# Kernel optimization log

Measured on AMD Instinct MI355X. Metric: run time of the kernel, lower is better.

The kernel has to match this reference:

```python
import jax, jax.numpy as jnp
import numpy as np
import math

D_MODEL = 512
D_STATE = 16
D_CONV = 4
EXPAND = 2
D_INNER = EXPAND * D_MODEL          # 1024
D_HALF = D_INNER // 2               # 512, channels for x and z branches
DT_RANK = math.ceil(D_MODEL / 16)   # 32
B_SZ, L_SEQ = 8, 4096


def _dwconv_same(x, kern):
    """Depthwise 1D conv, TF 'same' padding, stride 1.
    x: (b, d, l); kern: (d, k). Returns (b, d, l)."""
    d = x.shape[1]
    w = kern[:, None, :]  # (O=d, I=1, K)
    return jax.lax.conv_general_dilated(
        x, w, window_strides=(1,), padding='SAME',
        dimension_numbers=('NCH', 'OIH', 'NCH'), feature_group_count=d)


def setup_inputs() -> dict:
    key = jax.random.key(0)
    ks = jax.random.split(key, 10)
    hidden_states = jax.random.normal(ks[0], (B_SZ, L_SEQ, D_MODEL), jnp.float32)
    W_in = jax.random.normal(ks[1], (D_MODEL, D_INNER), jnp.float32) * (D_MODEL ** -0.5)
    W_xproj = jax.random.normal(ks[2], (D_HALF, DT_RANK + 2 * D_STATE), jnp.float32) * (D_HALF ** -0.5)
    dt_init_std = DT_RANK ** -0.5
    W_dt = jax.random.uniform(ks[3], (DT_RANK, D_HALF), jnp.float32, -dt_init_std, dt_init_std)
    # bias init: inverse softplus of dt ~ LogUniform(1e-3, 0.1)
    dt = jnp.exp(jax.random.uniform(ks[4], (D_HALF,), jnp.float32,
                                    math.log(1e-3), math.log(0.1)))
    dt = jnp.clip(dt, 1e-4, 0.1)
    b_dt = dt + jnp.log(-jnp.expm1(-dt))
    A_log = jnp.log(jnp.broadcast_to(jnp.arange(1, D_STATE + 1, dtype=jnp.float32),
                                     (D_HALF, D_STATE)))
    D = jnp.ones((D_HALF,), jnp.float32)
    K_x = jax.random.normal(ks[5], (D_HALF, D_CONV), jnp.float32) * (D_CONV ** -0.5)
    K_z = jax.random.normal(ks[6], (D_HALF, D_CONV), jnp.float32) * (D_CONV ** -0.5)
    W_out = jax.random.normal(ks[7], (D_INNER, D_MODEL), jnp.float32) * (D_INNER ** -0.5)
    return {"hidden_states": hidden_states, "W_in": W_in, "W_xproj": W_xproj,
            "W_dt": W_dt, "b_dt": b_dt, "A_log": A_log, "D": D,
            "K_x": K_x, "K_z": K_z, "W_out": W_out}


def reference(hidden_states, W_in, W_xproj, W_dt, b_dt, A_log, D, K_x, K_z, W_out):
    r, n = W_dt.shape[0], A_log.shape[1]
    b, l, _ = hidden_states.shape
    xz = hidden_states @ W_in                         # (b,l,2d)
    x, z = jnp.split(xz, 2, axis=-1)                  # (b,l,d) each
    x = jax.nn.silu(_dwconv_same(x.transpose(0, 2, 1), K_x)).transpose(0, 2, 1)
    z = jax.nn.silu(_dwconv_same(z.transpose(0, 2, 1), K_z)).transpose(0, 2, 1)
    x_dbl = x @ W_xproj                               # (b,l,r+2n)
    delta = jax.nn.softplus(x_dbl[..., :r] @ W_dt + b_dt)   # (b,l,d)
    Bm = x_dbl[..., r:r + n]                          # (b,l,n)
    Cm = x_dbl[..., r + n:]                           # (b,l,n)
    A = -jnp.exp(A_log)                               # (d,n)

    def step(h, inp):
        x_t, d_t, B_t, C_t = inp                      # (b,d),(b,d),(b,n),(b,n)
        dA = jnp.exp(d_t[:, :, None] * A)             # (b,d,n)
        h = h * dA + (d_t * x_t)[:, :, None] * B_t[:, None, :]
        y_t = jnp.einsum('bdn,bn->bd', h, C_t)
        return h, y_t

    xs = (x.transpose(1, 0, 2), delta.transpose(1, 0, 2),
          Bm.transpose(1, 0, 2), Cm.transpose(1, 0, 2))
    h0 = jnp.zeros((b, x.shape[-1], n), x.dtype)
    _, ys = jax.lax.scan(step, h0, xs)                # (l,b,d)
    y = ys.transpose(1, 0, 2) + x * D                 # skip term D*x
    out = jnp.concatenate([y, z], axis=-1) @ W_out    # (b,l,d_model)
    return out
```

## Files before the change

### kernel.cpp

```cpp
#include <hip/hip_runtime.h>
#include <hip/hip_bf16.h>
#include <cstdint>
#include <cstddef>

#define B_SZ    8
#define L_SEQ   4096
#define D_MODEL 512
#define D_INNER 1024
#define D_HALF  512
#define DT_RANK 32
#define N_STATE 16
#define M_ROWS  (B_SZ * L_SEQ)
#define N_CHUNK 64
#define L_CHK   64

typedef __hip_bfloat16 bf16;
typedef __attribute__((ext_vector_type(8))) short bf16x8;
typedef __attribute__((ext_vector_type(4))) float f32x4;

__device__ __forceinline__ void unpack8(uint4 v, float* f) {
  f[0] = __uint_as_float(v.x << 16); f[1] = __uint_as_float(v.x & 0xffff0000u);
  f[2] = __uint_as_float(v.y << 16); f[3] = __uint_as_float(v.y & 0xffff0000u);
  f[4] = __uint_as_float(v.z << 16); f[5] = __uint_as_float(v.z & 0xffff0000u);
  f[6] = __uint_as_float(v.w << 16); f[7] = __uint_as_float(v.w & 0xffff0000u);
}
__device__ __forceinline__ unsigned pack2(float a, float b) {
  bf16 ha = __float2bfloat16(a), hb = __float2bfloat16(b);
  return (unsigned)*(const unsigned short*)&ha |
         ((unsigned)*(const unsigned short*)&hb << 16);
}

typedef __attribute__((address_space(1))) const void gas_void;
typedef __attribute__((address_space(3))) void las_void;
__device__ __forceinline__ void gload_lds16(const void* g, void* l) {
  __builtin_amdgcn_global_load_lds((gas_void*)g, (las_void*)l, 16, 0, 0);
}

template <bool AF32>
__global__ __launch_bounds__(256)
void gemm_mfma(const void* __restrict__ A1v, const bf16* __restrict__ A2,
               const bf16* __restrict__ BT, bf16* __restrict__ C,
               float* __restrict__ Cf, int N, int K) {
  __shared__ bf16 As[2][128 * 32];
  __shared__ bf16 Bs[2][128 * 32];
  const int tid  = threadIdx.x;
  const int bm   = blockIdx.x * 128;
  const int bn   = blockIdx.y * 128;
  const int wave = tid >> 6;
  const int lane = tid & 63;
  const int wm   = (wave & 1) * 64;
  const int wn   = (wave >> 1) * 64;
  const int l15  = lane & 15;
  const int quad = lane >> 4;
  const int lr   = lane >> 2;
  const int lc   = (lane & 3) * 8;

  f32x4 acc[4][4] = {};
  const int NT = K >> 5;

  auto stage = [&](int buf, int t) {
    const int k0 = t * 32;
#pragma unroll
    for (int p = 0; p < 2; ++p) {
      const int c = wave + p * 4;
      gload_lds16(&BT[(size_t)(bn + c * 16 + lr) * K + k0 + lc],
                  &Bs[buf][c * 16 * 32]);
    }
    if constexpr (AF32) {
      const float* Ap = (const float*)A1v;
      const int sr0 = tid >> 2;
      const int sc  = (tid & 3) * 8;
#pragma unroll
      for (int p = 0; p < 2; ++p) {
        const int r = sr0 + p * 64;
        const float* s = &Ap[(size_t)(bm + r) * 512 + k0 + sc];
        const float4 v0 = *(const float4*)s;
        const float4 v1 = *(const float4*)(s + 4);
        uint4 o;
        o.x = pack2(v0.x, v0.y); o.y = pack2(v0.z, v0.w);
        o.z = pack2(v1.x, v1.y); o.w = pack2(v1.z, v1.w);
        *(uint4*)&As[buf][r * 32 + sc] = o;
      }
    } else {
      const bf16* Ap = (k0 < 512) ? (const bf16*)A1v : A2;
      const int ka = k0 & 511;
#pragma unroll
      for (int p = 0; p < 2; ++p) {
        const int c = wave + p * 4;
        gload_lds16(&Ap[(size_t)(bm + c * 16 + lr) * 512 + ka + lc],
                    &As[buf][c * 16 * 32]);
      }
    }
  };

  stage(0, 0);
  __syncthreads();
  int cur = 0;
  for (int t = 0; t < NT; ++t) {
    if (t + 1 < NT) stage(cur ^ 1, t + 1);
    bf16x8 af[4], bfr[4];
#pragma unroll
    for (int i = 0; i < 4; ++i)
      af[i] = *(const bf16x8*)&As[cur][(wm + i * 16 + l15) * 32 + quad * 8];
#pragma unroll
    for (int j = 0; j < 4; ++j)
      bfr[j] = *(const bf16x8*)&Bs[cur][(wn + j * 16 + l15) * 32 + quad * 8];
#pragma unroll
    for (int i = 0; i < 4; ++i)
#pragma unroll
      for (int j = 0; j < 4; ++j)
        acc[i][j] = __builtin_amdgcn_mfma_f32_16x16x32_bf16(
            af[i], bfr[j], acc[i][j], 0, 0, 0);
    __syncthreads();
    cur ^= 1;
  }

  if (Cf) {
#pragma unroll
    for (int i = 0; i < 4; ++i)
#pragma unroll
      for (int j = 0; j < 4; ++j)
#pragma unroll
        for (int r = 0; r < 4; ++r) {
          const int row = bm + wm + i * 16 + quad * 4 + r;
          const int col = bn + wn + j * 16 + l15;
          Cf[(size_t)row * N + col] = acc[i][j][r];
        }
  } else {
#pragma unroll
    for (int i = 0; i < 4; ++i)
#pragma unroll
      for (int j = 0; j < 4; ++j)
#pragma unroll
        for (int r = 0; r < 4; ++r) {
          const int row = bm + wm + i * 16 + quad * 4 + r;
          const int col = bn + wn + j * 16 + l15;
          C[(size_t)row * N + col] = __float2bfloat16(acc[i][j][r]);
        }
  }
}

__global__ __launch_bounds__(256)
void gemm_xproj(const bf16* __restrict__ A, const bf16* __restrict__ BT,
                float* __restrict__ C, bf16* __restrict__ dtA) {
  __shared__ bf16 As[2][128 * 32];
  __shared__ bf16 Bs[2][64 * 32];
  const int tid  = threadIdx.x;
  const int bm   = blockIdx.x * 128;
  const int wave = tid >> 6;
  const int lane = tid & 63;
  const int wm   = (wave & 1) * 64;
  const int wn   = (wave >> 1) * 32;
  const int l15  = lane & 15;
  const int quad = lane >> 4;
  const int lr   = lane >> 2;
  const int lc   = (lane & 3) * 8;

  f32x4 acc[4][2] = {};

  auto stage = [&](int buf, int t) {
    const int k0 = t * 32;
#pragma unroll
    for (int p = 0; p < 2; ++p) {
      const int c = wave + p * 4;
      gload_lds16(&A[(size_t)(bm + c * 16 + lr) * 512 + k0 + lc],
                  &As[buf][c * 16 * 32]);
    }
    gload_lds16(&BT[(size_t)(wave * 16 + lr) * 512 + k0 + lc],
                &Bs[buf][wave * 16 * 32]);
  };

  stage(0, 0);
  __syncthreads();
  int cur = 0;
  for (int t = 0; t < 16; ++t) {
    if (t + 1 < 16) stage(cur ^ 1, t + 1);
    bf16x8 af[4], bfr[2];
#pragma unroll
    for (int i = 0; i < 4; ++i)
      af[i] = *(const bf16x8*)&As[cur][(wm + i * 16 + l15) * 32 + quad * 8];
#pragma unroll
    for (int j = 0; j < 2; ++j)
      bfr[j] = *(const bf16x8*)&Bs[cur][(wn + j * 16 + l15) * 32 + quad * 8];
#pragma unroll
    for (int i = 0; i < 4; ++i)
#pragma unroll
      for (int j = 0; j < 2; ++j)
        acc[i][j] = __builtin_amdgcn_mfma_f32_16x16x32_bf16(
            af[i], bfr[j], acc[i][j], 0, 0, 0);
    __syncthreads();
    cur ^= 1;
  }

#pragma unroll
  for (int i = 0; i < 4; ++i)
#pragma unroll
    for (int j = 0; j < 2; ++j)
#pragma unroll
      for (int r = 0; r < 4; ++r) {
        const int row = bm + wm + i * 16 + quad * 4 + r;
        const int col = wn + j * 16 + l15;
        const float v = acc[i][j][r];
        C[(size_t)row * 64 + col] = v;
        if (wn == 0) {
          bf16 hi = __float2bfloat16(v);
          const float lo = v - __bfloat162float(hi);
          bf16 lob = __float2bfloat16(lo);
          unsigned short* dp = (unsigned short*)dtA + (size_t)row * 64 + col;
          dp[0]  = *(const unsigned short*)&hi;
          dp[32] = *(const unsigned short*)&lob;
        }
      }
}

__global__ __launch_bounds__(256)
void conv_silu(const bf16* __restrict__ P, const float* __restrict__ Kx,
               const float* __restrict__ Kz, bf16* __restrict__ Xc,
               bf16* __restrict__ Zc) {
  const unsigned g = blockIdx.x * 256 + threadIdx.x;
  const int d8   = (int)(g & 63) * 8;
  const int half = (int)(g >> 6) & 1;
  const int t0   = (int)((g >> 7) & 511) * 8;
  const int b    = (int)(g >> 16);

  const float* Kf = half ? Kz : Kx;
  float k[8][4];
#pragma unroll
  for (int u = 0; u < 8; ++u) {
    const float4 v = *(const float4*)&Kf[(d8 + u) * 4];
    k[u][0] = v.x; k[u][1] = v.y; k[u][2] = v.z; k[u][3] = v.w;
  }

  const bf16* src = P + (size_t)b * L_SEQ * 1024 + half * 512 + d8;
  bf16* dst = (half ? Zc : Xc) + ((size_t)b * L_SEQ + t0) * 512 + d8;

  uint4 p[11];
#pragma unroll
  for (int i = 0; i < 11; ++i) {
    const int t = t0 + i - 1;
    p[i] = (t >= 0 && t < L_SEQ) ? *(const uint4*)&src[(size_t)t * 1024]
                                 : make_uint4(0u, 0u, 0u, 0u);
  }

#pragma unroll
  for (int i = 0; i < 8; ++i) {
    float r0[8], r1[8], r2[8], r3[8];
    unpack8(p[i],     r0);
    unpack8(p[i + 1], r1);
    unpack8(p[i + 2], r2);
    unpack8(p[i + 3], r3);
    float s[8];
#pragma unroll
    for (int u = 0; u < 8; ++u) {
      float a = r0[u] * k[u][0];
      a = fmaf(r1[u], k[u][1], a);
      a = fmaf(r2[u], k[u][2], a);
      a = fmaf(r3[u], k[u][3], a);
      s[u] = a / (1.f + __expf(-a));
    }
    uint4 o;
    o.x = pack2(s[0], s[1]); o.y = pack2(s[2], s[3]);
    o.z = pack2(s[4], s[5]); o.w = pack2(s[6], s[7]);
    *(uint4*)&dst[(size_t)i * 512] = o;
  }
}

__global__ __launch_bounds__(256)
void cvt_wdtT(const float* __restrict__ Wdt, bf16* __restrict__ WdtT) {
  const int n = blockIdx.x * 256 + threadIdx.x;
  unsigned short hbuf[32];
#pragma unroll
  for (int kk = 0; kk < 32; ++kk) {
    bf16 h = __float2bfloat16(Wdt[kk * 512 + n]);
    hbuf[kk] = *(const unsigned short*)&h;
  }
  unsigned short* o = (unsigned short*)WdtT + (size_t)n * 64;
#pragma unroll
  for (int kk = 0; kk < 32; ++kk) { o[kk] = hbuf[kk]; o[32 + kk] = hbuf[kk]; }
}

__global__ __launch_bounds__(256)
void delta_mfma(const bf16* __restrict__ A, const bf16* __restrict__ BT,
                const float* __restrict__ bdt, bf16* __restrict__ delta) {
  __shared__ bf16 As[128 * 32];
  __shared__ bf16 Bs[128 * 32];
  const int tid  = threadIdx.x;
  const int bm   = blockIdx.x * 128;
  const int bn   = blockIdx.y * 128;
  const int wave = tid >> 6;
  const int lane = tid & 63;
  const int wm   = (wave & 1) * 64;
  const int wn   = (wave >> 1) * 64;
  const int l15  = lane & 15;
  const int quad = lane >> 4;
  const int sr0  = tid >> 2;
  const int sc   = (tid & 3) * 8;

  f32x4 acc[4][4] = {};

  for (int k0 = 0; k0 < 64; k0 += 32) {
#pragma unroll
    for (int p = 0; p < 2; ++p) {
      const int r = sr0 + p * 64;
      *(uint4*)&As[r * 32 + sc] =
          *(const uint4*)&A[(size_t)(bm + r) * 64 + k0 + sc];
      *(uint4*)&Bs[r * 32 + sc] =
          *(const uint4*)&BT[(size_t)(bn + r) * 64 + k0 + sc];
    }
    __syncthreads();
    bf16x8 af[4], bfr[4];
#pragma unroll
    for (int i = 0; i < 4; ++i)
      af[i] = *(const bf16x8*)&As[(wm + i * 16 + l15) * 32 + quad * 8];
#pragma unroll
    for (int j = 0; j < 4; ++j)
      bfr[j] = *(const bf16x8*)&Bs[(wn + j * 16 + l15) * 32 + quad * 8];
#pragma unroll
    for (int i = 0; i < 4; ++i)
#pragma unroll
      for (int j = 0; j < 4; ++j)
        acc[i][j] = __builtin_amdgcn_mfma_f32_16x16x32_bf16(
            af[i], bfr[j], acc[i][j], 0, 0, 0);
    __syncthreads();
  }

#pragma unroll
  for (int j = 0; j < 4; ++j) {
    const int col = bn + wn + j * 16 + l15;
    const float bb = bdt[col];
#pragma unroll
    for (int i = 0; i < 4; ++i)
#pragma unroll
      for (int r = 0; r < 4; ++r) {
        const int row = bm + wm + i * 16 + quad * 4 + r;
        float v = acc[i][j][r] + bb;
        v = (v > 15.f) ? v : __logf(1.f + __expf(v));
        delta[(size_t)row * 512 + col] = __float2bfloat16(v);
      }
  }
}

__global__ __launch_bounds__(256)
void transpose_w_cvt(const float* __restrict__ W, bf16* __restrict__ WT,
                     int K, int N) {
  __shared__ float tile[64][65];
  const int kb = blockIdx.x * 64;
  const int nb = blockIdx.y * 64;
  const int c4 = (threadIdx.x & 15) * 4;
  const int r0 = threadIdx.x >> 4;
#pragma unroll
  for (int p = 0; p < 4; ++p) {
    const int r = r0 + p * 16;
    *(float4*)&tile[r][c4] = *(const float4*)&W[(size_t)(kb + r) * N + nb + c4];
  }
  __syncthreads();
#pragma unroll
  for (int p = 0; p < 4; ++p) {
    const int n = r0 + p * 16;
    unsigned short tmp[4];
#pragma unroll
    for (int j = 0; j < 4; ++j) {
      bf16 h = __float2bfloat16(tile[c4 + j][n]);
      tmp[j] = *(unsigned short*)&h;
    }
    *(uint2*)&((unsigned short*)WT)[(size_t)(nb + n) * K + kb + c4] =
        *(const uint2*)tmp;
  }
}

__global__ __launch_bounds__(256)
void scan_pass_a(const bf16* __restrict__ Xc, const bf16* __restrict__ delta,
                 const float* __restrict__ xdbl, const float* __restrict__ A_log,
                 float* __restrict__ AC, float* __restrict__ HC) {
  const int d = blockIdx.x * 256 + threadIdx.x;
  const int b = blockIdx.y;
  const int c = blockIdx.z;

  float Acoef[16];
  {
    const float4* a4 = (const float4*)(A_log + (size_t)d * 16);
#pragma unroll
    for (int q = 0; q < 4; ++q) {
      const float4 v = a4[q];
      Acoef[q * 4 + 0] = -__expf(v.x);
      Acoef[q * 4 + 1] = -__expf(v.y);
      Acoef[q * 4 + 2] = -__expf(v.z);
      Acoef[q * 4 + 3] = -__expf(v.w);
    }
  }

  const size_t mrow = (size_t)b * L_SEQ + (size_t)c * L_CHK;
  const bf16* xp = Xc    + mrow * 512 + d;
  const bf16* dp = delta + mrow * 512 + d;
  const float* xr = xdbl + mrow * 64;

  float h[16];
#pragma unroll
  for (int n = 0; n < 16; ++n) h[n] = 0.f;
  float S = 0.f;

  for (int t0 = 0; t0 < L_CHK; t0 += 4) {
    float dtv[4], xv[4];
#pragma unroll
    for (int i = 0; i < 4; ++i) {
      dtv[i] = __bfloat162float(dp[(size_t)(t0 + i) * 512]);
      xv[i]  = __bfloat162float(xp[(size_t)(t0 + i) * 512]);
    }
#pragma unroll
    for (int i = 0; i < 4; ++i) {
      const float dt  = dtv[i];
      const float dtx = dt * xv[i];
      const float* r  = xr + (size_t)(t0 + i) * 64;
      S += dt;
#pragma unroll
      for (int n = 0; n < 16; ++n) {
        const float dA = __expf(dt * Acoef[n]);
        h[n] = fmaf(h[n], dA, dtx * r[32 + n]);
      }
    }
  }

  const size_t idx = (((size_t)c * B_SZ + b) * 512 + d) * 16;
  float4* acp = (float4*)(AC + idx);
  float4* hcp = (float4*)(HC + idx);
#pragma unroll
  for (int q = 0; q < 4; ++q) {
    acp[q] = make_float4(__expf(Acoef[q * 4 + 0] * S),
                         __expf(Acoef[q * 4 + 1] * S),
                         __expf(Acoef[q * 4 + 2] * S),
                         __expf(Acoef[q * 4 + 3] * S));
    hcp[q] = make_float4(h[q * 4 + 0], h[q * 4 + 1],
                         h[q * 4 + 2], h[q * 4 + 3]);
  }
}

__global__ __launch_bounds__(256)
void scan_combine(const float* __restrict__ AC, float* __restrict__ HC) {
  const size_t idx = (size_t)blockIdx.x * 256 + threadIdx.x;
  float hi = 0.f;
  for (int c = 0; c < N_CHUNK; ++c) {
    const size_t o = (size_t)c * 65536 + idx;
    const float tmp = HC[o];
    HC[o] = hi;
    hi = fmaf(AC[o], hi, tmp);
  }
}

__global__ __launch_bounds__(256)
void scan_pass_b(bf16* __restrict__ XY, const bf16* __restrict__ delta,
                 const float* __restrict__ xdbl, const float* __restrict__ A_log,
                 const float* __restrict__ Dvec, const float* __restrict__ HC) {
  const int d = blockIdx.x * 256 + threadIdx.x;
  const int b = blockIdx.y;
  const int c = blockIdx.z;

  float Acoef[16];
  {
    const float4* a4 = (const float4*)(A_log + (size_t)d * 16);
#pragma unroll
    for (int q = 0; q < 4; ++q) {
      const float4 v = a4[q];
      Acoef[q * 4 + 0] = -__expf(v.x);
      Acoef[q * 4 + 1] = -__expf(v.y);
      Acoef[q * 4 + 2] = -__expf(v.z);
      Acoef[q * 4 + 3] = -__expf(v.w);
    }
  }
  const float Dv = Dvec[d];

  const size_t mrow = (size_t)b * L_SEQ + (size_t)c * L_CHK;
  bf16*       xp = XY + mrow * 512 + d;
  const bf16* dp = delta + mrow * 512 + d;
  const float* xr = xdbl + mrow * 64;

  float h[16];
  {
    const size_t idx = (((size_t)c * B_SZ + b) * 512 + d) * 16;
    const float4* hcp = (const float4*)(HC + idx);
#pragma unroll
    for (int q = 0; q < 4; ++q) {
      const float4 v = hcp[q];
      h[q * 4 + 0] = v.x; h[q * 4 + 1] = v.y;
      h[q * 4 + 2] = v.z; h[q * 4 + 3] = v.w;
    }
  }

  for (int t0 = 0; t0 < L_CHK; t0 += 4) {
    float dtv[4], xv[4];
#pragma unroll
    for (int i = 0; i < 4; ++i) {
      dtv[i] = __bfloat162float(dp[(size_t)(t0 + i) * 512]);
      xv[i]  = __bfloat162float(xp[(size_t)(t0 + i) * 512]);
    }
#pragma unroll
    for (int i = 0; i < 4; ++i) {
      const float dt  = dtv[i];
      const float dtx = dt * xv[i];
      const float* r  = xr + (size_t)(t0 + i) * 64;
#pragma unroll
      for (int n = 0; n < 16; ++n) {
        const float dA = __expf(dt * Acoef[n]);
        h[n] = fmaf(h[n], dA, dtx * r[32 + n]);
      }
      float y = xv[i] * Dv;
#pragma unroll
      for (int n = 0; n < 16; ++n) y = fmaf(h[n], r[48 + n], y);
      xp[(size_t)(t0 + i) * 512] = __float2bfloat16(y);
    }
  }
}

__global__ __launch_bounds__(256)
void diag_kernel(float* __restrict__ out, float code) {
  const size_t id = (size_t)blockIdx.x * 256 + threadIdx.x;
  out[id] = (id == 0) ? code : 0.f;
}

extern "C" void kernel_launch(void* const* d_in, const int* in_sizes, int n_in,
                              void* d_out, int out_size, void* d_ws, size_t ws_size,
                              hipStream_t stream) {
  const float* hidden  = (const float*)d_in[0];
  const float* W_in    = (const float*)d_in[1];
  const float* W_xproj = (const float*)d_in[2];
  const float* W_dt    = (const float*)d_in[3];
  const float* b_dt    = (const float*)d_in[4];
  const float* A_log   = (const float*)d_in[5];
  const float* Dvec    = (const float*)d_in[6];
  const float* K_x     = (const float*)d_in[7];
  const float* K_z     = (const float*)d_in[8];
  const float* W_out   = (const float*)d_in[9];
  float* out = (float*)d_out;

  const size_t MB = 1024 * 1024;
  if (ws_size < 72 * MB) {
    diag_kernel<<<dim3((M_ROWS * 512) / 256), dim3(256), 0, stream>>>(
        out, 1000.f + (float)(ws_size / MB));
    return;
  }

  uint8_t* w8 = (uint8_t*)d_ws;
  uint8_t* o8 = (uint8_t*)d_out;
  bf16*  Xc      = (bf16*)w8;
  bf16*  Zc      = (bf16*)(w8 + 32 * MB);
  bf16*  W_inT   = (bf16*)(w8 + 64 * MB);
  float* xdbl    = (float*)(w8 + 64 * MB);
  bf16*  W_outT  = (bf16*)(w8 + 64 * MB);
  bf16*  P       = (bf16*)o8;
  bf16*  delta   = (bf16*)o8;
  bf16*  W_xprojT= (bf16*)(o8 + 32 * MB);
  bf16*  dtA     = (bf16*)(o8 + 48 * MB);
  bf16*  WdtT    = (bf16*)(o8 + 52 * MB);
  float* AC      = (float*)(o8 + 32 * MB);
  float* HC      = (float*)(o8 + 48 * MB);

  dim3 blk(256);

  transpose_w_cvt<<<dim3(512 / 64, 1024 / 64), blk, 0, stream>>>(
      W_in, W_inT, 512, 1024);

  gemm_mfma<true><<<dim3(M_ROWS / 128, D_INNER / 128), blk, 0, stream>>>(
      hidden, nullptr, W_inT, P, nullptr, D_INNER, 512);

  conv_silu<<<dim3(2048), blk, 0, stream>>>(P, K_x, K_z, Xc, Zc);

  transpose_w_cvt<<<dim3(512 / 64, 64 / 64), blk, 0, stream>>>(
      W_xproj, W_xprojT, 512, 64);
  cvt_wdtT<<<dim3(2), blk, 0, stream>>>(W_dt, WdtT);
  gemm_xproj<<<dim3(M_ROWS / 128), blk, 0, stream>>>(Xc, W_xprojT, xdbl, dtA);

  delta_mfma<<<dim3(M_ROWS / 128, 512 / 128), blk, 0, stream>>>(
      dtA, WdtT, b_dt, delta);

  scan_pass_a<<<dim3(2, B_SZ, N_CHUNK), blk, 0, stream>>>(
      Xc, delta, xdbl, A_log, AC, HC);
  scan_combine<<<dim3(65536 / 256), blk, 0, stream>>>(AC, HC);
  scan_pass_b<<<dim3(2, B_SZ, N_CHUNK), blk, 0, stream>>>(
      Xc, delta, xdbl, A_log, Dvec, HC);

  transpose_w_cvt<<<dim3(1024 / 64, 512 / 64), blk, 0, stream>>>(
      W_out, W_outT, 1024, 512);

  gemm_mfma<false><<<dim3(M_ROWS / 128, D_MODEL / 128), blk, 0, stream>>>(
      Xc, Zc, W_outT, nullptr, out, D_MODEL, 1024);
}
```

Measured before the change: 401.3 us.

## Deepen GEMM LDS pipeline to four stages and pre-convert input to bf16

Both MFMA GEMM kernels move from a double-buffered LDS pipeline to a 4-slot ring with three tiles in flight. Each iteration now uses explicit vmcnt waits and a single barrier in place of a trailing __syncthreads, so global-to-LDS loads overlap the MFMA work more. The fp32 hidden states are converted to bf16 by a separate kernel, which lets the input-projection GEMM use async global_load_lds for its A operand as well. In exchange, LDS per block doubles, which may reduce occupancy, and the extra conversion pass adds memory traffic.

Measured after the change: 412.2 us. +2.7%, slower.

```diff
diff --git a/kernel.cpp b/kernel.cpp
--- a/kernel.cpp
+++ b/kernel.cpp
@@ -36,13 +36,12 @@
   __builtin_amdgcn_global_load_lds((gas_void*)g, (las_void*)l, 16, 0, 0);
 }
 
-template <bool AF32>
-__global__ __launch_bounds__(256)
-void gemm_mfma(const void* __restrict__ A1v, const bf16* __restrict__ A2,
+__global__ __launch_bounds__(256)
+void gemm_mfma(const bf16* __restrict__ A1, const bf16* __restrict__ A2,
                const bf16* __restrict__ BT, bf16* __restrict__ C,
                float* __restrict__ Cf, int N, int K) {
-  __shared__ bf16 As[2][128 * 32];
-  __shared__ bf16 Bs[2][128 * 32];
+  __shared__ bf16 As[4][128 * 32];
+  __shared__ bf16 Bs[4][128 * 32];
   const int tid  = threadIdx.x;
   const int bm   = blockIdx.x * 128;
   const int bn   = blockIdx.y * 128;
@@ -60,44 +59,27 @@
 
   auto stage = [&](int buf, int t) {
     const int k0 = t * 32;
+    const bf16* Ap = (k0 < 512) ? A1 : A2;
+    const int ka = k0 & 511;
 #pragma unroll
     for (int p = 0; p < 2; ++p) {
       const int c = wave + p * 4;
+      gload_lds16(&Ap[(size_t)(bm + c * 16 + lr) * 512 + ka + lc],
+                  &As[buf][c * 16 * 32]);
       gload_lds16(&BT[(size_t)(bn + c * 16 + lr) * K + k0 + lc],
                   &Bs[buf][c * 16 * 32]);
     }
-    if constexpr (AF32) {
-      const float* Ap = (const float*)A1v;
-      const int sr0 = tid >> 2;
-      const int sc  = (tid & 3) * 8;
-#pragma unroll
-      for (int p = 0; p < 2; ++p) {
-        const int r = sr0 + p * 64;
-        const float* s = &Ap[(size_t)(bm + r) * 512 + k0 + sc];
-        const float4 v0 = *(const float4*)s;
-        const float4 v1 = *(const float4*)(s + 4);
-        uint4 o;
-        o.x = pack2(v0.x, v0.y); o.y = pack2(v0.z, v0.w);
-        o.z = pack2(v1.x, v1.y); o.w = pack2(v1.z, v1.w);
-        *(uint4*)&As[buf][r * 32 + sc] = o;
-      }
-    } else {
-      const bf16* Ap = (k0 < 512) ? (const bf16*)A1v : A2;
-      const int ka = k0 & 511;
-#pragma unroll
-      for (int p = 0; p < 2; ++p) {
-        const int c = wave + p * 4;
-        gload_lds16(&Ap[(size_t)(bm + c * 16 + lr) * 512 + ka + lc],
-                    &As[buf][c * 16 * 32]);
-      }
-    }
   };
 
-  stage(0, 0);
-  __syncthreads();
-  int cur = 0;
+  stage(0, 0); stage(1, 1); stage(2, 2);
+
   for (int t = 0; t < NT; ++t) {
-    if (t + 1 < NT) stage(cur ^ 1, t + 1);
+    if (t < NT - 2)       asm volatile("s_waitcnt vmcnt(8)" ::: "memory");
+    else if (t == NT - 2) asm volatile("s_waitcnt vmcnt(4)" ::: "memory");
+    else                  asm volatile("s_waitcnt vmcnt(0)" ::: "memory");
+    __builtin_amdgcn_s_barrier();
+    __builtin_amdgcn_sched_barrier(0);
+    const int cur = t & 3;
     bf16x8 af[4], bfr[4];
 #pragma unroll
     for (int i = 0; i < 4; ++i)
@@ -105,14 +87,13 @@
 #pragma unroll
     for (int j = 0; j < 4; ++j)
       bfr[j] = *(const bf16x8*)&Bs[cur][(wn + j * 16 + l15) * 32 + quad * 8];
+    if (t + 3 < NT) stage((t + 3) & 3, t + 3);
 #pragma unroll
     for (int i = 0; i < 4; ++i)
 #pragma unroll
       for (int j = 0; j < 4; ++j)
         acc[i][j] = __builtin_amdgcn_mfma_f32_16x16x32_bf16(
             af[i], bfr[j], acc[i][j], 0, 0, 0);
-    __syncthreads();
-    cur ^= 1;
   }
 
   if (Cf) {
@@ -143,8 +124,8 @@
 __global__ __launch_bounds__(256)
 void gemm_xproj(const bf16* __restrict__ A, const bf16* __restrict__ BT,
                 float* __restrict__ C, bf16* __restrict__ dtA) {
-  __shared__ bf16 As[2][128 * 32];
-  __shared__ bf16 Bs[2][64 * 32];
+  __shared__ bf16 As[4][128 * 32];
+  __shared__ bf16 Bs[4][64 * 32];
   const int tid  = threadIdx.x;
   const int bm   = blockIdx.x * 128;
   const int wave = tid >> 6;
@@ -170,11 +151,15 @@
                 &Bs[buf][wave * 16 * 32]);
   };
 
-  stage(0, 0);
-  __syncthreads();
-  int cur = 0;
+  stage(0, 0); stage(1, 1); stage(2, 2);
+
   for (int t = 0; t < 16; ++t) {
-    if (t + 1 < 16) stage(cur ^ 1, t + 1);
+    if (t < 14)       asm volatile("s_waitcnt vmcnt(6)" ::: "memory");
+    else if (t == 14) asm volatile("s_waitcnt vmcnt(3)" ::: "memory");
+    else              asm volatile("s_waitcnt vmcnt(0)" ::: "memory");
+    __builtin_amdgcn_s_barrier();
+    __builtin_amdgcn_sched_barrier(0);
+    const int cur = t & 3;
     bf16x8 af[4], bfr[2];
 #pragma unroll
     for (int i = 0; i < 4; ++i)
@@ -182,14 +167,13 @@
 #pragma unroll
     for (int j = 0; j < 2; ++j)
       bfr[j] = *(const bf16x8*)&Bs[cur][(wn + j * 16 + l15) * 32 + quad * 8];
+    if (t + 3 < 16) stage((t + 3) & 3, t + 3);
 #pragma unroll
     for (int i = 0; i < 4; ++i)
 #pragma unroll
       for (int j = 0; j < 2; ++j)
         acc[i][j] = __builtin_amdgcn_mfma_f32_16x16x32_bf16(
             af[i], bfr[j], acc[i][j], 0, 0, 0);
-    __syncthreads();
-    cur ^= 1;
   }
 
 #pragma unroll
@@ -369,6 +353,17 @@
 }
 
 __global__ __launch_bounds__(256)
+void cvt_f32_bf16(const float* __restrict__ I, bf16* __restrict__ O) {
+  const size_t id = ((size_t)blockIdx.x * 256 + threadIdx.x) * 8;
+  const float4 v0 = *(const float4*)(I + id);
+  const float4 v1 = *(const float4*)(I + id + 4);
+  uint4 o;
+  o.x = pack2(v0.x, v0.y); o.y = pack2(v0.z, v0.w);
+  o.z = pack2(v1.x, v1.y); o.w = pack2(v1.z, v1.w);
+  *(uint4*)((unsigned short*)O + id) = o;
+}
+
+__global__ __launch_bounds__(256)
 void scan_pass_a(const bf16* __restrict__ Xc, const bf16* __restrict__ delta,
                  const float* __restrict__ xdbl, const float* __restrict__ A_log,
                  float* __restrict__ AC, float* __restrict__ HC) {
@@ -540,6 +535,7 @@
 
   uint8_t* w8 = (uint8_t*)d_ws;
   uint8_t* o8 = (uint8_t*)d_out;
+  bf16*  hb      = (bf16*)w8;
   bf16*  Xc      = (bf16*)w8;
   bf16*  Zc      = (bf16*)(w8 + 32 * MB);
   bf16*  W_inT   = (bf16*)(w8 + 64 * MB);
@@ -555,11 +551,12 @@
 
   dim3 blk(256);
 
+  cvt_f32_bf16<<<dim3((M_ROWS * 512) / 2048), blk, 0, stream>>>(hidden, hb);
   transpose_w_cvt<<<dim3(512 / 64, 1024 / 64), blk, 0, stream>>>(
       W_in, W_inT, 512, 1024);
 
-  gemm_mfma<true><<<dim3(M_ROWS / 128, D_INNER / 128), blk, 0, stream>>>(
-      hidden, nullptr, W_inT, P, nullptr, D_INNER, 512);
+  gemm_mfma<<<dim3(M_ROWS / 128, D_INNER / 128), blk, 0, stream>>>(
+      hb, nullptr, W_inT, P, nullptr, D_INNER, 512);
 
   conv_silu<<<dim3(2048), blk, 0, stream>>>(P, K_x, K_z, Xc, Zc);
 
@@ -580,6 +577,6 @@
   transpose_w_cvt<<<dim3(1024 / 64, 512 / 64), blk, 0, stream>>>(
       W_out, W_outT, 1024, 512);
 
-  gemm_mfma<false><<<dim3(M_ROWS / 128, D_MODEL / 128), blk, 0, stream>>>(
+  gemm_mfma<<<dim3(M_ROWS / 128, D_MODEL / 128), blk, 0, stream>>>(
       Xc, Zc, W_outT, nullptr, out, D_MODEL, 1024);
 }
```
